# Performance work log

Measured on AMD Instinct MI355X. Metric: run time of the kernel, lower is better.

The kernel has to match this reference:

```python
import jax, jax.numpy as jnp
import numpy as np

KINEMATIC_CHAIN = [[0, 2, 5, 8, 11], [0, 1, 4, 7, 10], [0, 3, 6, 9, 12, 15],
                   [9, 14, 17, 19, 21], [9, 13, 16, 18, 20]]
PATHS = [c[1:] for c in KINEMATIC_CHAIN]  # paths = chain[1:] per gauss_integral_motion
FRAMES, JOINTS = 16384, 22


def setup_inputs() -> dict:
    key = jax.random.key(0)
    k1, k2 = jax.random.split(key)
    motion1 = jax.random.normal(k1, (FRAMES, JOINTS, 3), dtype=jnp.float32)
    motion2 = jax.random.normal(k2, (FRAMES, JOINTS, 3), dtype=jnp.float32)
    return {"motion1": motion1, "motion2": motion2}


def _safe_normalize(v):
    # vec / norm(vec) if norm != 0 else zeros  (matches the torch list comp)
    n = jnp.linalg.norm(v, axis=-1, keepdims=True)
    return jnp.where(n > 0, v / jnp.where(n > 0, n, 1.0), 0.0)


def _gli_pair(p1, p2):
    """Sum of Gauss link integrals over all segment pairs of two paths.
    p1: (L1, 3), p2: (L2, 3) -> scalar. Vectorized over the (L1-1, L2-1) segment grid."""
    s1, e1 = p1[:-1, None, :], p1[1:, None, :]   # (n1, 1, 3)
    s2, e2 = p2[None, :-1, :], p2[None, 1:, :]   # (1, n2, 3)
    r13, r14 = s2 - s1, e2 - s1
    r23, r24 = s2 - e1, e2 - e1
    r12, r34 = e1 - s1, e2 - s2
    faces = [jnp.cross(r13, r14), jnp.cross(r14, r24),
             jnp.cross(r24, r23), jnp.cross(r23, r13)]
    nf = [_safe_normalize(f) for f in faces]
    gli = jnp.zeros(jnp.broadcast_shapes(r13.shape[:-1], r24.shape[:-1]), p1.dtype)
    for i in range(4):
        d = jnp.clip(jnp.sum(nf[i] * nf[(i + 1) % 4], axis=-1), -1.0, 1.0)
        gli = gli + jnp.arcsin(d)
    sign = jnp.sum(jnp.cross(r34, r12) * r13, axis=-1)
    gli = gli * jnp.where(sign > 0, 1.0, -1.0) / (4.0 * jnp.pi)
    return jnp.sum(gli)


def _window_mask(motion1, motion2):
    # xz bounding-box overlap per frame, then dilate each contiguous run by 1
    # frame on each side (start = count-1, end = count+1-1 in the torch code).
    def bbox(m):  # (F, J, 3) -> min/max over joints of x and z
        x, z = m[..., 0], m[..., 2]
        return x.min(1), x.max(1), z.min(1), z.max(1)
    x1n, x1x, z1n, z1x = bbox(motion1)
    x2n, x2x, z2n, z2x = bbox(motion2)
    ov_x = ~((x1x < x2n) | (x2x < x1n))
    ov_z = ~((z1x < z2n) | (z2x < z1n))
    f = ov_x & ov_z  # (F,) bool
    false1 = jnp.zeros((1,), dtype=bool)
    prev = jnp.concatenate([false1, f[:-1]])
    nxt = jnp.concatenate([f[1:], false1])
    return f | prev | nxt


def _gli_motion(motion1, motion2):
    frame = motion1.shape[0]
    n_paths = len(PATHS)
    mask = _window_mask(motion1, motion2).astype(motion1.dtype)  # (F,)
    # GLI_motion[i, a, b]: vmap each path-pair over frames (25 fixed pairs)
    rows = []
    for pa in PATHS:
        p1 = motion1[:, jnp.asarray(pa), :]  # (F, La, 3)
        cols = []
        for pb in PATHS:
            p2 = motion2[:, jnp.asarray(pb), :]  # (F, Lb, 3)
            cols.append(jax.vmap(_gli_pair)(p1, p2))  # (F,)
        rows.append(jnp.stack(cols, axis=-1))  # (F, n_paths)
    gli = jnp.stack(rows, axis=-2)  # (F, n_paths, n_paths)
    gli = gli * mask[:, None, None]  # frames outside windows stay zero
    vel = jnp.abs(gli[1:] - gli[:-1]).reshape(frame - 1, n_paths * n_paths)
    return jnp.max(vel, axis=1)  # (F-1,)


def reference(motion1, motion2):
    return _gli_motion(motion1, motion2)
```

## Files before the change

### kernel.cpp

```cpp
#include <hip/hip_runtime.h>
#include <math.h>

#define NFRAMES 16384
#define NJOINTS 22
#define NPATHS  5
#define NPAIRS  (NPATHS * NPATHS)
#define NSEG    16
#define GSTRIDE 32
#define FSTR    (NJOINTS * 3)
#define FPB     8

typedef float v2f __attribute__((ext_vector_type(2)));

__constant__ int2 c_seg[NSEG] = {
    {6,15},{15,24},{24,33},
    {3,12},{12,21},{21,30},
    {9,18},{18,27},{27,36},{36,45},
    {42,51},{51,57},{57,63},
    {39,48},{48,54},{54,60}
};
__constant__ int c_pstart[NPATHS] = {0, 3, 6, 10, 13};
__constant__ int c_plen[NPATHS]   = {3, 3, 4, 3, 3};

struct V3 { v2f x, y, z; };
__device__ __forceinline__ V3 vsub(V3 a, V3 b) { V3 r; r.x=a.x-b.x; r.y=a.y-b.y; r.z=a.z-b.z; return r; }
__device__ __forceinline__ v2f vdot(V3 a, V3 b) { return a.x*b.x + a.y*b.y + a.z*b.z; }
__device__ __forceinline__ V3 vcross(V3 a, V3 b) {
    V3 r;
    r.x = a.y*b.z - a.z*b.y;
    r.y = a.z*b.x - a.x*b.z;
    r.z = a.x*b.y - a.y*b.x;
    return r;
}

__device__ __forceinline__ v2f vfast_asin(v2f x) {
    v2f a = __builtin_elementwise_max(x, -x);
    v2f p = a * -0.0187293f + 0.0742610f;
    p = a * p + -0.2121144f;
    p = a * p + 1.5707288f;
    v2f s;
    s.x = __builtin_amdgcn_sqrtf(1.0f - a.x);
    s.y = __builtin_amdgcn_sqrtf(1.0f - a.y);
    v2f r = 1.5707963268f - s * p;
    r.x = (x.x < 0.0f) ? -r.x : r.x;
    r.y = (x.y < 0.0f) ? -r.y : r.y;
    return r;
}

__device__ __forceinline__ v2f vasin_term(v2f d, v2f ma, v2f mb) {
    v2f m = ma * mb;
    v2f rs;
    rs.x = __builtin_amdgcn_rsqf(m.x);
    rs.y = __builtin_amdgcn_rsqf(m.y);
    v2f one = 1.0f, mone = -1.0f;
    v2f x = __builtin_elementwise_min(one, __builtin_elementwise_max(mone, d * rs));
    v2f r = vfast_asin(x);
    r.x = (ma.x > 0.0f && mb.x > 0.0f) ? r.x : 0.0f;
    r.y = (ma.y > 0.0f && mb.y > 0.0f) ? r.y : 0.0f;
    return r;
}

__device__ __forceinline__ v2f shfl_xor_v2(v2f v, int mask, int width) {
    v2f r;
    r.x = __shfl_xor(v.x, mask, width);
    r.y = __shfl_xor(v.y, mask, width);
    return r;
}

__global__ __launch_bounds__(256) void k_gli(const float* __restrict__ m1,
                                             const float* __restrict__ m2,
                                             float* __restrict__ gli,
                                             int* __restrict__ ov) {
    __shared__ v2f sF[4][2 * FSTR];
    __shared__ v2f sT[4][260];

    int t = threadIdx.x;
    int w = t >> 6;
    int l = t & 63;
    int fp = blockIdx.x * FPB + 2 * w;
    const float* a = m1 + (size_t)fp * FSTR;
    const float* b = m2 + (size_t)fp * FSTR;

    v2f* sFw = sF[w];
    float* sFf = (float*)sFw;

    {
        int u1 = l + 64;
        int fr1 = (u1 >= FSTR) ? 1 : 0;
        int co1 = u1 - fr1 * FSTR;
        float a0v = a[l], a1v = a[u1];
        float b0v = b[l], b1v = b[u1];
        sFf[2 * l] = a0v;
        sFf[2 * co1 + fr1] = a1v;
        sFf[2 * FSTR + 2 * l] = b0v;
        sFf[2 * FSTR + 2 * co1 + fr1] = b1v;
        if (l < 2 * FSTR - 128) {
            int u2 = l + 128;
            int co2 = u2 - FSTR;
            sFf[2 * co2 + 1] = a[u2];
            sFf[2 * FSTR + 2 * co2 + 1] = b[u2];
        }
        if (l == 32) sT[w][256] = v2f{0.0f, 0.0f};
    }
    __syncthreads();

    {
        int j = l & 15;
        int i0 = l >> 4;
        int2 o2 = c_seg[j];
        const v2f* B = sFw + FSTR;
        V3 s2; s2.x = B[o2.x]; s2.y = B[o2.x+1]; s2.z = B[o2.x+2];
        V3 e2; e2.x = B[o2.y]; e2.y = B[o2.y+1]; e2.z = B[o2.y+2];
        V3 r34 = vsub(e2, s2);
        for (int k = 0; k < 4; k++) {
            int2 o1 = c_seg[i0 + 4 * k];
            V3 s1; s1.x = sFw[o1.x]; s1.y = sFw[o1.x+1]; s1.z = sFw[o1.x+2];
            V3 e1; e1.x = sFw[o1.y]; e1.y = sFw[o1.y+1]; e1.z = sFw[o1.y+2];

            V3 r12 = vsub(e1, s1);
            V3 r13 = vsub(s2, s1);
            V3 r14 = vsub(e2, s1);

            V3 f0v = vcross(r13, r14);
            V3 c1  = vcross(r12, r13);
            V3 c2  = vcross(r12, r14);
            V3 f2  = vsub(vsub(c2, c1), f0v);

            v2f q0 = vdot(f0v, f0v);
            v2f q1 = vdot(c2, c2);
            v2f q2 = vdot(f2, f2);
            v2f q3 = vdot(c1, c1);

            v2f g = vasin_term( vdot(f0v, c2), q0, q1)
                  + vasin_term( vdot(c2, f2),  q1, q2)
                  + vasin_term(-vdot(f2, c1),  q2, q3)
                  + vasin_term(-vdot(c1, f0v), q3, q0);

            v2f sg = -vdot(c2, r13);
            v2f res;
            res.x = (sg.x > 0.0f) ? g.x : -g.x;
            res.y = (sg.y > 0.0f) ? g.y : -g.y;
            sT[w][l + 64 * k] = res;
        }
        (void)r34;
    }

    {
        int half = l >> 5;
        int jj = l & 31;
        if (jj > NJOINTS - 1) jj = NJOINTS - 1;
        const v2f* p = sFw + half * FSTR;
        v2f x = p[jj * 3 + 0];
        v2f z = p[jj * 3 + 2];
        v2f xn = x, xx = x, zn = z, zx = z;
#pragma unroll
        for (int k = 1; k < 32; k <<= 1) {
            xn = __builtin_elementwise_min(xn, shfl_xor_v2(xn, k, 32));
            xx = __builtin_elementwise_max(xx, shfl_xor_v2(xx, k, 32));
            zn = __builtin_elementwise_min(zn, shfl_xor_v2(zn, k, 32));
            zx = __builtin_elementwise_max(zx, shfl_xor_v2(zx, k, 32));
        }
        v2f oxn = shfl_xor_v2(xn, 32, 64);
        v2f oxx = shfl_xor_v2(xx, 32, 64);
        v2f ozn = shfl_xor_v2(zn, 32, 64);
        v2f ozx = shfl_xor_v2(zx, 32, 64);
        if (l == 0) {
            int2 o;
            bool vx0 = !((xx.x < oxn.x) || (oxx.x < xn.x));
            bool vz0 = !((zx.x < ozn.x) || (ozx.x < zn.x));
            bool vx1 = !((xx.y < oxn.y) || (oxx.y < xn.y));
            bool vz1 = !((zx.y < ozn.y) || (ozx.y < zn.y));
            o.x = (vx0 && vz0) ? 1 : 0;
            o.y = (vx1 && vz1) ? 1 : 0;
            *(int2*)(ov + fp) = o;
        }
    }
    __syncthreads();

    if (l < NPAIRS) {
        int pa = (l * 205) >> 10;
        int pb = l - pa * 5;
        int ia0 = c_pstart[pa], na = c_plen[pa];
        int ib0 = c_pstart[pb], nb = c_plen[pb];
        v2f s = v2f{0.0f, 0.0f};
#pragma unroll
        for (int ka = 0; ka < 4; ka++) {
#pragma unroll
            for (int kb = 0; kb < 4; kb++) {
                int idx = (ka < na && kb < nb) ? ((ia0 + ka) * 16 + (ib0 + kb)) : 256;
                s += sT[w][idx];
            }
        }
        s *= 0.07957747154594767f;
        gli[(size_t)fp * GSTRIDE + l] = s.x;
        gli[(size_t)(fp + 1) * GSTRIDE + l] = s.y;
    }
}

__global__ void k_out(const float* __restrict__ gli, const int* __restrict__ ov,
                      float* __restrict__ out) {
    int f = blockIdx.x * blockDim.x + threadIdx.x;
    if (f >= NFRAMES - 1) return;

    int m0 = ov[f];
    if (f > 0) m0 |= ov[f - 1];
    m0 |= ov[f + 1];

    int m1 = ov[f + 1] | ov[f];
    if (f + 2 <= NFRAMES - 1) m1 |= ov[f + 2];

    float ma = m0 ? 1.0f : 0.0f;
    float mb = m1 ? 1.0f : 0.0f;

    const float4* g0v = (const float4*)(gli + (size_t)f * GSTRIDE);
    const float4* g1v = (const float4*)(gli + (size_t)(f + 1) * GSTRIDE);
    float v = 0.0f;
#pragma unroll
    for (int q = 0; q < 6; q++) {
        float4 u0 = g0v[q];
        float4 u1 = g1v[q];
        v = fmaxf(v, fabsf(u1.x * mb - u0.x * ma));
        v = fmaxf(v, fabsf(u1.y * mb - u0.y * ma));
        v = fmaxf(v, fabsf(u1.z * mb - u0.z * ma));
        v = fmaxf(v, fabsf(u1.w * mb - u0.w * ma));
    }
    {
        float u0 = ((const float*)g0v)[24];
        float u1 = ((const float*)g1v)[24];
        v = fmaxf(v, fabsf(u1 * mb - u0 * ma));
    }
    out[f] = v;
}

extern "C" void kernel_launch(void* const* d_in, const int* in_sizes, int n_in,
                              void* d_out, int out_size, void* d_ws, size_t ws_size,
                              hipStream_t stream) {
    const float* m1 = (const float*)d_in[0];
    const float* m2 = (const float*)d_in[1];
    float* out = (float*)d_out;

    float* gli = (float*)d_ws;
    int* ov = (int*)(gli + (size_t)NFRAMES * GSTRIDE);

    k_gli<<<NFRAMES / FPB, 256, 0, stream>>>(m1, m2, gli, ov);

    {
        int threads = 256;
        int blocks = (NFRAMES - 1 + threads - 1) / threads;
        k_out<<<blocks, threads, 0, stream>>>(gli, ov, out);
    }
}
```

Baseline: 79.47 us.

## Fuse GLI computation and velocity-max output into one kernel with halo frames

Merges the per-frame GLI kernel and the output kernel into one 512-thread block that handles 16 frames: 13 output frames plus halo frames on each side. The mask, GLI values and frame differences stay in shared memory, so the global workspace round trip and the second launch are gone. In exchange, 3 of every 16 frames are computed twice, which adds about 23% more GLI arithmetic. Blocks are also larger and need more shared memory.

```diff
diff --git a/kernel.cpp b/kernel.cpp
--- a/kernel.cpp
+++ b/kernel.cpp
@@ -6,9 +6,10 @@
 #define NPATHS  5
 #define NPAIRS  (NPATHS * NPATHS)
 #define NSEG    16
-#define GSTRIDE 32
 #define FSTR    (NJOINTS * 3)
-#define FPB     8
+#define OPB     13
+#define LFR     16
+#define GLS     26
 
 typedef float v2f __attribute__((ext_vector_type(2)));
 
@@ -67,38 +68,42 @@
     return r;
 }
 
-__global__ __launch_bounds__(256) void k_gli(const float* __restrict__ m1,
-                                             const float* __restrict__ m2,
-                                             float* __restrict__ gli,
-                                             int* __restrict__ ov) {
-    __shared__ v2f sF[4][2 * FSTR];
-    __shared__ v2f sT[4][260];
+__global__ __launch_bounds__(512) void k_fused(const float* __restrict__ m1,
+                                               const float* __restrict__ m2,
+                                               float* __restrict__ out) {
+    __shared__ v2f sF[8][2 * FSTR];
+    __shared__ v2f sT[8][257];
+    __shared__ float gl[LFR * GLS];
+    __shared__ int ovl[LFR];
 
     int t = threadIdx.x;
     int w = t >> 6;
     int l = t & 63;
-    int fp = blockIdx.x * FPB + 2 * w;
-    const float* a = m1 + (size_t)fp * FSTR;
-    const float* b = m2 + (size_t)fp * FSTR;
+    int s = (int)blockIdx.x * OPB - 1;
+    int fA = s + 2 * w;
+    int fB = fA + 1;
+    int fAc = fA < 0 ? 0 : (fA > NFRAMES - 1 ? NFRAMES - 1 : fA);
+    int fBc = fB < 0 ? 0 : (fB > NFRAMES - 1 ? NFRAMES - 1 : fB);
 
     v2f* sFw = sF[w];
     float* sFf = (float*)sFw;
 
-    {
-        int u1 = l + 64;
-        int fr1 = (u1 >= FSTR) ? 1 : 0;
-        int co1 = u1 - fr1 * FSTR;
-        float a0v = a[l], a1v = a[u1];
-        float b0v = b[l], b1v = b[u1];
-        sFf[2 * l] = a0v;
-        sFf[2 * co1 + fr1] = a1v;
-        sFf[2 * FSTR + 2 * l] = b0v;
-        sFf[2 * FSTR + 2 * co1 + fr1] = b1v;
-        if (l < 2 * FSTR - 128) {
-            int u2 = l + 128;
-            int co2 = u2 - FSTR;
-            sFf[2 * co2 + 1] = a[u2];
-            sFf[2 * FSTR + 2 * co2 + 1] = b[u2];
+    const float* aA = m1 + (size_t)fAc * FSTR;
+    const float* aB = m1 + (size_t)fBc * FSTR;
+    const float* bA = m2 + (size_t)fAc * FSTR;
+    const float* bB = m2 + (size_t)fBc * FSTR;
+
+    {
+        sFf[2 * l]     = aA[l];
+        sFf[2 * l + 1] = aB[l];
+        sFf[2 * (FSTR + l)]     = bA[l];
+        sFf[2 * (FSTR + l) + 1] = bB[l];
+        if (l < FSTR - 64) {
+            int c = l + 64;
+            sFf[2 * c]     = aA[c];
+            sFf[2 * c + 1] = aB[c];
+            sFf[2 * (FSTR + c)]     = bA[c];
+            sFf[2 * (FSTR + c) + 1] = bB[c];
         }
         if (l == 32) sT[w][256] = v2f{0.0f, 0.0f};
     }
@@ -111,7 +116,6 @@
         const v2f* B = sFw + FSTR;
         V3 s2; s2.x = B[o2.x]; s2.y = B[o2.x+1]; s2.z = B[o2.x+2];
         V3 e2; e2.x = B[o2.y]; e2.y = B[o2.y+1]; e2.z = B[o2.y+2];
-        V3 r34 = vsub(e2, s2);
         for (int k = 0; k < 4; k++) {
             int2 o1 = c_seg[i0 + 4 * k];
             V3 s1; s1.x = sFw[o1.x]; s1.y = sFw[o1.x+1]; s1.z = sFw[o1.x+2];
@@ -142,7 +146,6 @@
             res.y = (sg.y > 0.0f) ? g.y : -g.y;
             sT[w][l + 64 * k] = res;
         }
-        (void)r34;
     }
 
     {
@@ -165,14 +168,12 @@
         v2f ozn = shfl_xor_v2(zn, 32, 64);
         v2f ozx = shfl_xor_v2(zx, 32, 64);
         if (l == 0) {
-            int2 o;
             bool vx0 = !((xx.x < oxn.x) || (oxx.x < xn.x));
             bool vz0 = !((zx.x < ozn.x) || (ozx.x < zn.x));
             bool vx1 = !((xx.y < oxn.y) || (oxx.y < xn.y));
             bool vz1 = !((zx.y < ozn.y) || (ozx.y < zn.y));
-            o.x = (vx0 && vz0) ? 1 : 0;
-            o.y = (vx1 && vz1) ? 1 : 0;
-            *(int2*)(ov + fp) = o;
+            ovl[2 * w]     = (fA >= 0 && fA < NFRAMES && vx0 && vz0) ? 1 : 0;
+            ovl[2 * w + 1] = (fB >= 0 && fB < NFRAMES && vx1 && vz1) ? 1 : 0;
         }
     }
     __syncthreads();
@@ -182,54 +183,40 @@
         int pb = l - pa * 5;
         int ia0 = c_pstart[pa], na = c_plen[pa];
         int ib0 = c_pstart[pb], nb = c_plen[pb];
-        v2f s = v2f{0.0f, 0.0f};
+        v2f sum = v2f{0.0f, 0.0f};
 #pragma unroll
         for (int ka = 0; ka < 4; ka++) {
 #pragma unroll
             for (int kb = 0; kb < 4; kb++) {
                 int idx = (ka < na && kb < nb) ? ((ia0 + ka) * 16 + (ib0 + kb)) : 256;
-                s += sT[w][idx];
+                sum += sT[w][idx];
             }
         }
-        s *= 0.07957747154594767f;
-        gli[(size_t)fp * GSTRIDE + l] = s.x;
-        gli[(size_t)(fp + 1) * GSTRIDE + l] = s.y;
-    }
-}
-
-__global__ void k_out(const float* __restrict__ gli, const int* __restrict__ ov,
-                      float* __restrict__ out) {
-    int f = blockIdx.x * blockDim.x + threadIdx.x;
-    if (f >= NFRAMES - 1) return;
-
-    int m0 = ov[f];
-    if (f > 0) m0 |= ov[f - 1];
-    m0 |= ov[f + 1];
-
-    int m1 = ov[f + 1] | ov[f];
-    if (f + 2 <= NFRAMES - 1) m1 |= ov[f + 2];
-
-    float ma = m0 ? 1.0f : 0.0f;
-    float mb = m1 ? 1.0f : 0.0f;
-
-    const float4* g0v = (const float4*)(gli + (size_t)f * GSTRIDE);
-    const float4* g1v = (const float4*)(gli + (size_t)(f + 1) * GSTRIDE);
-    float v = 0.0f;
-#pragma unroll
-    for (int q = 0; q < 6; q++) {
-        float4 u0 = g0v[q];
-        float4 u1 = g1v[q];
-        v = fmaxf(v, fabsf(u1.x * mb - u0.x * ma));
-        v = fmaxf(v, fabsf(u1.y * mb - u0.y * ma));
-        v = fmaxf(v, fabsf(u1.z * mb - u0.z * ma));
-        v = fmaxf(v, fabsf(u1.w * mb - u0.w * ma));
-    }
-    {
-        float u0 = ((const float*)g0v)[24];
-        float u1 = ((const float*)g1v)[24];
-        v = fmaxf(v, fabsf(u1 * mb - u0 * ma));
-    }
-    out[f] = v;
+        sum *= 0.07957747154594767f;
+        gl[(2 * w) * GLS + l]     = sum.x;
+        gl[(2 * w + 1) * GLS + l] = sum.y;
+    }
+    __syncthreads();
+
+    {
+        int h = t >> 5;
+        int j = t & 31;
+        int f = (int)blockIdx.x * OPB + h;
+        if (h < OPB && f <= NFRAMES - 2) {
+            int lf = h + 1;
+            int mm0 = ovl[lf - 1] | ovl[lf] | ovl[lf + 1];
+            int mm1 = ovl[lf] | ovl[lf + 1] | ovl[lf + 2];
+            float ma = mm0 ? 1.0f : 0.0f;
+            float mb = mm1 ? 1.0f : 0.0f;
+            float v = 0.0f;
+            if (j < NPAIRS)
+                v = fabsf(gl[(lf + 1) * GLS + j] * mb - gl[lf * GLS + j] * ma);
+#pragma unroll
+            for (int k = 1; k < 32; k <<= 1)
+                v = fmaxf(v, __shfl_xor(v, k, 32));
+            if (j == 0) out[f] = v;
+        }
+    }
 }
 
 extern "C" void kernel_launch(void* const* d_in, const int* in_sizes, int n_in,
@@ -239,14 +226,6 @@
     const float* m2 = (const float*)d_in[1];
     float* out = (float*)d_out;
 
-    float* gli = (float*)d_ws;
-    int* ov = (int*)(gli + (size_t)NFRAMES * GSTRIDE);
-
-    k_gli<<<NFRAMES / FPB, 256, 0, stream>>>(m1, m2, gli, ov);
-
-    {
-        int threads = 256;
-        int blocks = (NFRAMES - 1 + threads - 1) / threads;
-        k_out<<<blocks, threads, 0, stream>>>(gli, ov, out);
-    }
-}
+    int blocks = (NFRAMES - 1 + OPB - 1) / OPB;
+    k_fused<<<blocks, 512, 0, stream>>>(m1, m2, out);
+}
```

Result: no change. 79.58 us (+0.1%).
